# Performance work log

Hardware: AMD Instinct MI355X
Metric: run time of the kernel (lower is better)

The kernel has to match this reference:

```python
import jax, jax.numpy as jnp
import numpy as np

NUM_HEADS = 16
D_MODEL = 1024
D_K = 64
D_V = 64
B, S = 4, 2048
TEMPERATURE = float(np.sqrt(NUM_HEADS * D_K))  # module uses sqrt(H*d_k), not sqrt(d_k)


def setup_inputs() -> dict:
    key = jax.random.key(0)
    ks = jax.random.split(key, 7)
    q = jax.random.normal(ks[0], (B, S, D_MODEL), dtype=jnp.float32)
    k = jax.random.normal(ks[1], (B, S, D_MODEL), dtype=jnp.float32)
    v = jax.random.normal(ks[2], (B, S, D_MODEL), dtype=jnp.float32)
    # causal mask: True = masked out (matches torch masked_fill semantics)
    mask = jnp.broadcast_to(jnp.triu(jnp.ones((S, S), dtype=bool), k=1), (B, S, S))
    scale = 1.0 / np.sqrt(D_MODEL)
    Wq = jax.random.normal(ks[3], (D_MODEL, NUM_HEADS * D_K), dtype=jnp.float32) * scale
    Wk = jax.random.normal(ks[4], (D_MODEL, NUM_HEADS * D_K), dtype=jnp.float32) * scale
    Wv = jax.random.normal(ks[5], (D_MODEL, NUM_HEADS * D_V), dtype=jnp.float32) * scale
    Wo = jax.random.normal(ks[6], (NUM_HEADS * D_V, D_MODEL), dtype=jnp.float32) * scale
    return {"q": q, "k": k, "v": v, "mask": mask,
            "Wq": Wq, "Wk": Wk, "Wv": Wv, "Wo": Wo}


def _split_heads(x):
    # [B,S,H*d] -> [B,H,S,d]
    b, s, _ = x.shape
    return x.reshape(b, s, NUM_HEADS, -1).transpose(0, 2, 1, 3)


def reference(q, k, v, mask, Wq, Wk, Wv, Wo):
    qh = _split_heads(q @ Wq)   # [B,H,S,d_k]
    kh = _split_heads(k @ Wk)   # [B,H,S,d_k]
    vh = _split_heads(v @ Wv)   # [B,H,S,d_v]
    attn = jnp.einsum('bhqd,bhkd->bhqk', qh / TEMPERATURE, kh)
    attn = jnp.where(mask[:, None, :, :], -jnp.inf, attn)
    attn = jax.nn.softmax(attn, axis=-1)
    out = jnp.einsum('bhqk,bhkd->bhqd', attn, vh)  # [B,H,S,d_v]
    out = out.transpose(0, 2, 1, 3).reshape(q.shape[0], q.shape[1], -1)
    out = out @ Wo  # [B,S,d_model]
    return out, attn
```

## Files before the change

kernel.cpp:

```cpp
#include <hip/hip_runtime.h>
#include <hip/hip_bf16.h>
#include <math.h>

#define SLEN 2048
#define NB 4
#define NH 16
#define DM 1024
#define DH 64

typedef __attribute__((ext_vector_type(8))) short bf16x8;
typedef __attribute__((ext_vector_type(8))) unsigned short ushort8;
typedef __attribute__((ext_vector_type(4))) unsigned short ushort4v;
typedef __attribute__((ext_vector_type(4))) float f32x4;

#define MFMA16(a, b, c) __builtin_amdgcn_mfma_f32_16x16x32_bf16((a), (b), (c), 0, 0, 0)

__device__ __forceinline__ unsigned short f2b(float f) {
    unsigned u = __builtin_bit_cast(unsigned, f);
    u = (u + 0x7FFFu + ((u >> 16) & 1u)) >> 16;
    return (unsigned short)u;
}

__device__ __forceinline__ float b2f(unsigned short h) {
    return __builtin_bit_cast(float, (unsigned)h << 16);
}

__device__ __forceinline__ void gload16(const unsigned short* g, unsigned short* l) {
    __builtin_amdgcn_global_load_lds((const __attribute__((address_space(1))) unsigned int*)g,
                                     (__attribute__((address_space(3))) unsigned int*)l,
                                     16, 0, 0);
}

__global__ __launch_bounds__(256) void wtrans4(const float* __restrict__ w0,
                                               const float* __restrict__ w1,
                                               const float* __restrict__ w2,
                                               const float* __restrict__ w3,
                                               unsigned short* __restrict__ outBase) {
    int z = blockIdx.z;
    const float* in = (z == 0) ? w0 : (z == 1) ? w1 : (z == 2) ? w2 : w3;
    unsigned short* out = outBase + (size_t)z * DM * DM;
    float scale = (z == 0) ? (1.4426950408889634f / 32.f) : 1.f;
    __shared__ float tile[32][33];
    int k0 = blockIdx.y * 32, n0 = blockIdx.x * 32;
    int tx = threadIdx.x & 31, ty = threadIdx.x >> 5;
    for (int i = ty; i < 32; i += 8) tile[i][tx] = in[(size_t)(k0 + i) * DM + n0 + tx];
    __syncthreads();
    for (int i = ty; i < 32; i += 8) out[(size_t)(n0 + i) * DM + k0 + tx] = f2b(tile[tx][i] * scale);
}

__global__ __launch_bounds__(256) void cast3(const float* __restrict__ q,
                                             const float* __restrict__ k,
                                             const float* __restrict__ v,
                                             unsigned short* __restrict__ dstBase, int n8) {
    int z = blockIdx.z;
    const float* in = (z == 0) ? q : (z == 1) ? k : v;
    unsigned short* out = dstBase + (size_t)z * NB * SLEN * DM;
    int stride = gridDim.x * 256;
    for (int i = blockIdx.x * 256 + threadIdx.x; i < n8; i += stride) {
        float4 a = ((const float4*)in)[2 * i];
        float4 b = ((const float4*)in)[2 * i + 1];
        ushort8 h = {f2b(a.x), f2b(a.y), f2b(a.z), f2b(a.w),
                     f2b(b.x), f2b(b.y), f2b(b.z), f2b(b.w)};
        ((ushort8*)out)[i] = h;
    }
}

__global__ __launch_bounds__(256) void vtrans(const unsigned short* __restrict__ Vh,
                                              unsigned short* __restrict__ Vt) {
    int bh = blockIdx.y;
    int b = bh >> 4, h = bh & 15;
    int s0 = blockIdx.x * 64;
    __shared__ __align__(16) unsigned short tile[64][72];
    int t = threadIdx.x;
    int r = t >> 2, seg = (t & 3) * 16;
    const ushort8* src = (const ushort8*)&Vh[(size_t)(b * SLEN + s0 + r) * DM + h * 64 + seg];
    *(ushort8*)&tile[r][seg] = src[0];
    *(ushort8*)&tile[r][seg + 8] = src[1];
    __syncthreads();
    unsigned short tmp[16];
#pragma unroll
    for (int i = 0; i < 16; i++) tmp[i] = tile[seg + i][r];
    ushort8 o0, o1;
#pragma unroll
    for (int i = 0; i < 8; i++) { o0[i] = tmp[i]; o1[i] = tmp[8 + i]; }
    unsigned short* dst = &Vt[(size_t)(bh * 64 + r) * SLEN + s0 + seg];
    *(ushort8*)dst = o0;
    *(ushort8*)&dst[8] = o1;
}

template <bool OUT_F32>
__global__ __launch_bounds__(256) void gemm_mz(const unsigned short* __restrict__ A0, size_t sA,
                                               const unsigned short* __restrict__ B0, size_t sB,
                                               void* __restrict__ C0, size_t sC,
                                               int N, int K) {
    __shared__ __align__(16) unsigned short As[128 * 64];
    __shared__ __align__(16) unsigned short Bs[128 * 64];
    int bid = blockIdx.x;
    int z = bid >> 9, inner = bid & 511;
    const unsigned short* A = A0 + (size_t)z * sA;
    const unsigned short* Bt = B0 + (size_t)z * sB;
    int m0 = (inner >> 3) * 128, n0 = (inner & 7) * 128;
    int t = threadIdx.x, lane = t & 63, w = t >> 6;
    int wm = (w >> 1) * 64, wn = (w & 1) * 64;
    int lr = lane & 15, hi = lane >> 4, lk = hi * 8, lq = hi * 4;
    int srow = w * 8 + (lane >> 3);
    int scol = (lane & 7) * 8;
    f32x4 acc[4][4] = {};
    for (int kt = 0; kt < K; kt += 64) {
        __syncthreads();
#pragma unroll
        for (int c = 0; c < 4; c++) {
            int row = c * 32 + srow;
            gload16(&A[(size_t)(m0 + row) * K + kt + scol], &As[(c * 4 + w) * 512]);
            gload16(&Bt[(size_t)(n0 + row) * K + kt + scol], &Bs[(c * 4 + w) * 512]);
        }
        __syncthreads();
#pragma unroll
        for (int ks = 0; ks < 2; ks++) {
            bf16x8 a[4], b[4];
#pragma unroll
            for (int mt = 0; mt < 4; mt++) a[mt] = *(const bf16x8*)&As[(wm + mt * 16 + lr) * 64 + ks * 32 + lk];
#pragma unroll
            for (int nt = 0; nt < 4; nt++) b[nt] = *(const bf16x8*)&Bs[(wn + nt * 16 + lr) * 64 + ks * 32 + lk];
#pragma unroll
            for (int mt = 0; mt < 4; mt++)
#pragma unroll
                for (int nt = 0; nt < 4; nt++) acc[mt][nt] = MFMA16(a[mt], b[nt], acc[mt][nt]);
        }
    }
#pragma unroll
    for (int mt = 0; mt < 4; mt++)
#pragma unroll
        for (int nt = 0; nt < 4; nt++)
#pragma unroll
            for (int r = 0; r < 4; r++) {
                int rr = m0 + wm + mt * 16 + lq + r;
                int cc = n0 + wn + nt * 16 + lr;
                if constexpr (OUT_F32)
                    ((float*)C0 + (size_t)z * sC)[(size_t)rr * N + cc] = acc[mt][nt][r];
                else
                    ((unsigned short*)C0 + (size_t)z * sC)[(size_t)rr * N + cc] = f2b(acc[mt][nt][r]);
            }
}

__global__ __launch_bounds__(512) void attn_kernel(const unsigned short* __restrict__ Qh,
                                                   const unsigned short* __restrict__ Kh,
                                                   const unsigned short* __restrict__ Vt,
                                                   float* __restrict__ attn_out,
                                                   unsigned short* __restrict__ O) {
    int bx = blockIdx.x;
    int qt = bx >> 6, bh = bx & 63;
    int b = bh >> 4, h = bh & 15;
    int q0 = qt * 128;
    int t = threadIdx.x, lane = t & 63, w = t >> 6;
    int lr = lane & 15, hi = lane >> 4, lk = hi * 8, lq = hi * 4;
    __shared__ __align__(16) unsigned short Ks[2][64 * 72];
    __shared__ __align__(16) unsigned short Vs[64 * 72];
    __shared__ __align__(16) unsigned short Ps[8][16 * 72];

    int qrow = q0 + w * 16 + lr;
    bf16x8 aq0 = *(const bf16x8*)&Qh[(size_t)(b * SLEN + qrow) * DM + h * 64 + lk];
    bf16x8 aq1 = *(const bf16x8*)&Qh[(size_t)(b * SLEN + qrow) * DM + h * 64 + 32 + lk];

    int srow = t >> 3, sseg = (t & 7) * 8;
    int ntile = 2 * qt + 2;
    int nfull = (q0 + w * 16 + 1) >> 6;
    int nact  = ((q0 + w * 16 + 15) >> 6) + 1;
    const unsigned short* Kbase = &Kh[(size_t)(b * SLEN + srow) * DM + h * 64 + sseg];
    const unsigned short* Vbase = &Vt[(size_t)(bh * 64 + srow) * SLEN + sseg];

    float rowsum = 0.f;

    ushort8 kreg = *(const ushort8*)&Kbase[0];
    for (int j = 0; j < ntile; j++) {
        ushort8 knext{};
        if (j + 1 < ntile) knext = *(const ushort8*)&Kbase[(size_t)(j + 1) * 64 * DM];
        *(ushort8*)&Ks[j & 1][srow * 72 + sseg] = kreg;
        __syncthreads();
        kreg = knext;
        if (j < nact) {
            const unsigned short* Kb = Ks[j & 1];
            if (j < nfull) {
#pragma unroll
                for (int nt = 0; nt < 4; nt++) {
                    f32x4 acc = {0.f, 0.f, 0.f, 0.f};
                    bf16x8 b0 = *(const bf16x8*)&Kb[(nt * 16 + lr) * 72 + lk];
                    bf16x8 b1 = *(const bf16x8*)&Kb[(nt * 16 + lr) * 72 + 32 + lk];
                    acc = MFMA16(b0, aq0, acc);
                    acc = MFMA16(b1, aq1, acc);
#pragma unroll
                    for (int r = 0; r < 4; r++) rowsum += exp2f(acc[r]);
                }
            } else {
#pragma unroll
                for (int nt = 0; nt < 4; nt++) {
                    f32x4 acc = {0.f, 0.f, 0.f, 0.f};
                    bf16x8 b0 = *(const bf16x8*)&Kb[(nt * 16 + lr) * 72 + lk];
                    bf16x8 b1 = *(const bf16x8*)&Kb[(nt * 16 + lr) * 72 + 32 + lk];
                    acc = MFMA16(b0, aq0, acc);
                    acc = MFMA16(b1, aq1, acc);
#pragma unroll
                    for (int r = 0; r < 4; r++) {
                        int key = j * 64 + nt * 16 + lq + r;
                        if (key <= qrow) rowsum += exp2f(acc[r]);
                    }
                }
            }
        }
    }
    rowsum += __shfl_xor(rowsum, 16);
    rowsum += __shfl_xor(rowsum, 32);
    float nlg = -log2f(rowsum);
    f32x4 cinit = {nlg, nlg, nlg, nlg};

    f32x4 acco[4] = {};
    kreg = *(const ushort8*)&Kbase[0];
    ushort8 vreg = *(const ushort8*)&Vbase[0];
    for (int j = 0; j < ntile; j++) {
        ushort8 knext{}, vnext{};
        if (j + 1 < ntile) {
            knext = *(const ushort8*)&Kbase[(size_t)(j + 1) * 64 * DM];
            vnext = *(const ushort8*)&Vbase[(j + 1) * 64];
        }
        __syncthreads();
        *(ushort8*)&Ks[0][srow * 72 + sseg] = kreg;
        *(ushort8*)&Vs[srow * 72 + sseg] = vreg;
        __syncthreads();
        kreg = knext;
        vreg = vnext;
        if (j >= nact) continue;
        bool full = j < nfull;
#pragma unroll
        for (int nt = 0; nt < 4; nt++) {
            f32x4 acc = cinit;
            bf16x8 b0 = *(const bf16x8*)&Ks[0][(nt * 16 + lr) * 72 + lk];
            bf16x8 b1 = *(const bf16x8*)&Ks[0][(nt * 16 + lr) * 72 + 32 + lk];
            acc = MFMA16(b0, aq0, acc);
            acc = MFMA16(b1, aq1, acc);
            ushort4v pb;
            if (full) {
#pragma unroll
                for (int r = 0; r < 4; r++)
                    pb[r] = (unsigned short)(__builtin_bit_cast(unsigned, exp2f(acc[r])) >> 16);
            } else {
#pragma unroll
                for (int r = 0; r < 4; r++) {
                    int key = j * 64 + nt * 16 + lq + r;
                    float p = (key <= qrow) ? exp2f(acc[r]) : 0.f;
                    pb[r] = (unsigned short)(__builtin_bit_cast(unsigned, p) >> 16);
                }
            }
            *(ushort4v*)&Ps[w][lr * 72 + nt * 16 + lq] = pb;
        }
        {
            size_t abase = ((size_t)bh * SLEN + q0 + w * 16) * SLEN + j * 64 + lr * 4;
#pragma unroll
            for (int i = 0; i < 4; i++) {
                int row = i * 4 + hi;
                ushort4v pb4 = *(const ushort4v*)&Ps[w][row * 72 + lr * 4];
                f32x4 pf = {b2f(pb4[0]), b2f(pb4[1]), b2f(pb4[2]), b2f(pb4[3])};
                __builtin_nontemporal_store(pf, (f32x4*)&attn_out[abase + (size_t)row * SLEN]);
            }
        }
        bf16x8 pa0 = *(const bf16x8*)&Ps[w][lr * 72 + lk];
        bf16x8 pa1 = *(const bf16x8*)&Ps[w][lr * 72 + 32 + lk];
#pragma unroll
        for (int nt = 0; nt < 4; nt++) {
            bf16x8 bv0 = *(const bf16x8*)&Vs[(nt * 16 + lr) * 72 + lk];
            bf16x8 bv1 = *(const bf16x8*)&Vs[(nt * 16 + lr) * 72 + 32 + lk];
            acco[nt] = MFMA16(pa0, bv0, acco[nt]);
            acco[nt] = MFMA16(pa1, bv1, acco[nt]);
        }
    }

    int kz = nact * 64;
    if (kz < SLEN) {
        int n4 = (SLEN - kz) >> 2;
        f32x4 z4 = {0.f, 0.f, 0.f, 0.f};
        for (int rr = 0; rr < 16; rr++) {
            int qr = q0 + w * 16 + rr;
            f32x4* dst = (f32x4*)&attn_out[((size_t)bh * SLEN + qr) * SLEN + kz];
            for (int i = lane; i < n4; i += 64) __builtin_nontemporal_store(z4, &dst[i]);
        }
    }

#pragma unroll
    for (int nt = 0; nt < 4; nt++)
#pragma unroll
        for (int r = 0; r < 4; r++) {
            int qr = q0 + w * 16 + lq + r;
            O[(size_t)(b * SLEN + qr) * DM + h * 64 + nt * 16 + lr] = f2b(acco[nt][r]);
        }
}

extern "C" void kernel_launch(void* const* d_in, const int* in_sizes, int n_in,
                              void* d_out, int out_size, void* d_ws, size_t ws_size,
                              hipStream_t stream) {
    const float* q = (const float*)d_in[0];
    const float* k = (const float*)d_in[1];
    const float* v = (const float*)d_in[2];
    const float* Wq = (const float*)d_in[4];
    const float* Wk = (const float*)d_in[5];
    const float* Wv = (const float*)d_in[6];
    const float* Wo = (const float*)d_in[7];

    const size_t WSZ = (size_t)DM * DM;
    const size_t MSZ = (size_t)NB * SLEN * DM;

    unsigned short* WqT = (unsigned short*)d_ws;
    unsigned short* WoT = WqT + 3 * WSZ;
    unsigned short* Qh  = WqT + 4 * WSZ;
    unsigned short* Kh  = Qh + MSZ;
    unsigned short* Vh  = Kh + MSZ;
    unsigned short* Vt  = Vh + MSZ;
    unsigned short* O   = Vt + MSZ;

    float* out = (float*)d_out;
    float* attn = out + MSZ;
    unsigned short* Cq = (unsigned short*)attn;

    wtrans4<<<dim3(32, 32, 4), 256, 0, stream>>>(Wq, Wk, Wv, Wo, WqT);

    const int n8 = (int)(MSZ / 8);
    cast3<<<dim3(1024, 1, 3), 256, 0, stream>>>(q, k, v, Cq, n8);

    gemm_mz<false><<<1536, 256, 0, stream>>>(Cq, MSZ, WqT, WSZ, (void*)Qh, MSZ, DM, DM);

    vtrans<<<dim3(SLEN / 64, NB * NH), 256, 0, stream>>>(Vh, Vt);

    attn_kernel<<<NB * NH * (SLEN / 128), 512, 0, stream>>>(Qh, Kh, Vt, attn, O);

    gemm_mz<true><<<512, 256, 0, stream>>>(O, 0, WoT, 0, d_out, 0, DM, DM);
}
```

Before: 405.1 us.

## Load K and V MFMA fragments directly from global memory, dropping LDS staging

The attention kernel no longer stages K and V tiles through shared memory with block-wide barriers. Each wave now reads its MFMA operand fragments straight from global memory and loops only over its own active key tiles (nact) instead of the block-wide tile count. This removes the __syncthreads calls and the LDS traffic, and lets waves with fewer causal tiles finish early. The cost is that all 8 waves fetch the same K/V data separately, relying on the L1/L2 caches, and the loads are no longer prefetched a tile ahead.

```diff
diff --git a/kernel.cpp b/kernel.cpp
--- a/kernel.cpp
+++ b/kernel.cpp
@@ -154,56 +154,37 @@
     int q0 = qt * 128;
     int t = threadIdx.x, lane = t & 63, w = t >> 6;
     int lr = lane & 15, hi = lane >> 4, lk = hi * 8, lq = hi * 4;
-    __shared__ __align__(16) unsigned short Ks[2][64 * 72];
-    __shared__ __align__(16) unsigned short Vs[64 * 72];
     __shared__ __align__(16) unsigned short Ps[8][16 * 72];
 
     int qrow = q0 + w * 16 + lr;
     bf16x8 aq0 = *(const bf16x8*)&Qh[(size_t)(b * SLEN + qrow) * DM + h * 64 + lk];
     bf16x8 aq1 = *(const bf16x8*)&Qh[(size_t)(b * SLEN + qrow) * DM + h * 64 + 32 + lk];
 
-    int srow = t >> 3, sseg = (t & 7) * 8;
-    int ntile = 2 * qt + 2;
     int nfull = (q0 + w * 16 + 1) >> 6;
     int nact  = ((q0 + w * 16 + 15) >> 6) + 1;
-    const unsigned short* Kbase = &Kh[(size_t)(b * SLEN + srow) * DM + h * 64 + sseg];
-    const unsigned short* Vbase = &Vt[(size_t)(bh * 64 + srow) * SLEN + sseg];
+    const unsigned short* Kfrag = &Kh[(size_t)(b * SLEN + lr) * DM + h * 64 + lk];
+    const unsigned short* Vfrag = &Vt[(size_t)(bh * 64 + lr) * SLEN + lk];
 
     float rowsum = 0.f;
 
-    ushort8 kreg = *(const ushort8*)&Kbase[0];
-    for (int j = 0; j < ntile; j++) {
-        ushort8 knext{};
-        if (j + 1 < ntile) knext = *(const ushort8*)&Kbase[(size_t)(j + 1) * 64 * DM];
-        *(ushort8*)&Ks[j & 1][srow * 72 + sseg] = kreg;
-        __syncthreads();
-        kreg = knext;
-        if (j < nact) {
-            const unsigned short* Kb = Ks[j & 1];
-            if (j < nfull) {
-#pragma unroll
-                for (int nt = 0; nt < 4; nt++) {
-                    f32x4 acc = {0.f, 0.f, 0.f, 0.f};
-                    bf16x8 b0 = *(const bf16x8*)&Kb[(nt * 16 + lr) * 72 + lk];
-                    bf16x8 b1 = *(const bf16x8*)&Kb[(nt * 16 + lr) * 72 + 32 + lk];
-                    acc = MFMA16(b0, aq0, acc);
-                    acc = MFMA16(b1, aq1, acc);
-#pragma unroll
-                    for (int r = 0; r < 4; r++) rowsum += exp2f(acc[r]);
-                }
+    for (int j = 0; j < nact; j++) {
+        bool full = j < nfull;
+#pragma unroll
+        for (int nt = 0; nt < 4; nt++) {
+            const unsigned short* kp = &Kfrag[(size_t)(j * 64 + nt * 16) * DM];
+            bf16x8 b0 = *(const bf16x8*)kp;
+            bf16x8 b1 = *(const bf16x8*)&kp[32];
+            f32x4 acc = {0.f, 0.f, 0.f, 0.f};
+            acc = MFMA16(b0, aq0, acc);
+            acc = MFMA16(b1, aq1, acc);
+            if (full) {
+#pragma unroll
+                for (int r = 0; r < 4; r++) rowsum += exp2f(acc[r]);
             } else {
 #pragma unroll
-                for (int nt = 0; nt < 4; nt++) {
-                    f32x4 acc = {0.f, 0.f, 0.f, 0.f};
-                    bf16x8 b0 = *(const bf16x8*)&Kb[(nt * 16 + lr) * 72 + lk];
-                    bf16x8 b1 = *(const bf16x8*)&Kb[(nt * 16 + lr) * 72 + 32 + lk];
-                    acc = MFMA16(b0, aq0, acc);
-                    acc = MFMA16(b1, aq1, acc);
-#pragma unroll
-                    for (int r = 0; r < 4; r++) {
-                        int key = j * 64 + nt * 16 + lq + r;
-                        if (key <= qrow) rowsum += exp2f(acc[r]);
-                    }
+                for (int r = 0; r < 4; r++) {
+                    int key = j * 64 + nt * 16 + lq + r;
+                    if (key <= qrow) rowsum += exp2f(acc[r]);
                 }
             }
         }
@@ -214,27 +195,14 @@
     f32x4 cinit = {nlg, nlg, nlg, nlg};
 
     f32x4 acco[4] = {};
-    kreg = *(const ushort8*)&Kbase[0];
-    ushort8 vreg = *(const ushort8*)&Vbase[0];
-    for (int j = 0; j < ntile; j++) {
-        ushort8 knext{}, vnext{};
-        if (j + 1 < ntile) {
-            knext = *(const ushort8*)&Kbase[(size_t)(j + 1) * 64 * DM];
-            vnext = *(const ushort8*)&Vbase[(j + 1) * 64];
-        }
-        __syncthreads();
-        *(ushort8*)&Ks[0][srow * 72 + sseg] = kreg;
-        *(ushort8*)&Vs[srow * 72 + sseg] = vreg;
-        __syncthreads();
-        kreg = knext;
-        vreg = vnext;
-        if (j >= nact) continue;
+    for (int j = 0; j < nact; j++) {
         bool full = j < nfull;
 #pragma unroll
         for (int nt = 0; nt < 4; nt++) {
+            const unsigned short* kp = &Kfrag[(size_t)(j * 64 + nt * 16) * DM];
+            bf16x8 b0 = *(const bf16x8*)kp;
+            bf16x8 b1 = *(const bf16x8*)&kp[32];
             f32x4 acc = cinit;
-            bf16x8 b0 = *(const bf16x8*)&Ks[0][(nt * 16 + lr) * 72 + lk];
-            bf16x8 b1 = *(const bf16x8*)&Ks[0][(nt * 16 + lr) * 72 + 32 + lk];
             acc = MFMA16(b0, aq0, acc);
             acc = MFMA16(b1, aq1, acc);
             ushort4v pb;
@@ -266,8 +234,9 @@
         bf16x8 pa1 = *(const bf16x8*)&Ps[w][lr * 72 + 32 + lk];
 #pragma unroll
         for (int nt = 0; nt < 4; nt++) {
-            bf16x8 bv0 = *(const bf16x8*)&Vs[(nt * 16 + lr) * 72 + lk];
-            bf16x8 bv1 = *(const bf16x8*)&Vs[(nt * 16 + lr) * 72 + 32 + lk];
+            const unsigned short* vp = &Vfrag[(size_t)(nt * 16) * SLEN + j * 64];
+            bf16x8 bv0 = *(const bf16x8*)vp;
+            bf16x8 bv1 = *(const bf16x8*)&vp[32];
             acco[nt] = MFMA16(pa0, bv0, acco[nt]);
             acco[nt] = MFMA16(pa1, bv1, acco[nt]);
         }
```

Result: slower. 600.6 us (+48.3%).

## Fuse fp32-to-bf16 cast and V transpose into QKV projection GEMM

Applied to the files above, without the earlier changes.

Removes the separate cast kernel by having the QKV GEMM load fp32 activations, convert them to bf16 in registers and store them into shared memory, with register prefetch of the next K tile. For the V projection, MFMA operands are swapped so the output is written directly in transposed [h*64+d][b*S+s] layout, removing the vtrans kernel. The attention kernel's V addressing is updated to match. This cuts two launches and several full activation round-trips through memory. In exchange, the A loads now go through registers instead of direct-to-LDS loads, and the transposed V stores are strided.

```diff
diff --git a/kernel.cpp b/kernel.cpp
--- a/kernel.cpp
+++ b/kernel.cpp
@@ -48,57 +48,21 @@
     for (int i = ty; i < 32; i += 8) out[(size_t)(n0 + i) * DM + k0 + tx] = f2b(tile[tx][i] * scale);
 }
 
-__global__ __launch_bounds__(256) void cast3(const float* __restrict__ q,
-                                             const float* __restrict__ k,
-                                             const float* __restrict__ v,
-                                             unsigned short* __restrict__ dstBase, int n8) {
-    int z = blockIdx.z;
-    const float* in = (z == 0) ? q : (z == 1) ? k : v;
-    unsigned short* out = dstBase + (size_t)z * NB * SLEN * DM;
-    int stride = gridDim.x * 256;
-    for (int i = blockIdx.x * 256 + threadIdx.x; i < n8; i += stride) {
-        float4 a = ((const float4*)in)[2 * i];
-        float4 b = ((const float4*)in)[2 * i + 1];
-        ushort8 h = {f2b(a.x), f2b(a.y), f2b(a.z), f2b(a.w),
-                     f2b(b.x), f2b(b.y), f2b(b.z), f2b(b.w)};
-        ((ushort8*)out)[i] = h;
-    }
-}
-
-__global__ __launch_bounds__(256) void vtrans(const unsigned short* __restrict__ Vh,
-                                              unsigned short* __restrict__ Vt) {
-    int bh = blockIdx.y;
-    int b = bh >> 4, h = bh & 15;
-    int s0 = blockIdx.x * 64;
-    __shared__ __align__(16) unsigned short tile[64][72];
-    int t = threadIdx.x;
-    int r = t >> 2, seg = (t & 3) * 16;
-    const ushort8* src = (const ushort8*)&Vh[(size_t)(b * SLEN + s0 + r) * DM + h * 64 + seg];
-    *(ushort8*)&tile[r][seg] = src[0];
-    *(ushort8*)&tile[r][seg + 8] = src[1];
-    __syncthreads();
-    unsigned short tmp[16];
-#pragma unroll
-    for (int i = 0; i < 16; i++) tmp[i] = tile[seg + i][r];
-    ushort8 o0, o1;
-#pragma unroll
-    for (int i = 0; i < 8; i++) { o0[i] = tmp[i]; o1[i] = tmp[8 + i]; }
-    unsigned short* dst = &Vt[(size_t)(bh * 64 + r) * SLEN + s0 + seg];
-    *(ushort8*)dst = o0;
-    *(ushort8*)&dst[8] = o1;
-}
-
-template <bool OUT_F32>
-__global__ __launch_bounds__(256) void gemm_mz(const unsigned short* __restrict__ A0, size_t sA,
-                                               const unsigned short* __restrict__ B0, size_t sB,
-                                               void* __restrict__ C0, size_t sC,
-                                               int N, int K) {
+__global__ __launch_bounds__(256) void gemm_qkv(const float* __restrict__ Aq,
+                                                const float* __restrict__ Ak,
+                                                const float* __restrict__ Av,
+                                                const unsigned short* __restrict__ B0,
+                                                unsigned short* __restrict__ C0) {
+    const size_t WSZ = (size_t)DM * DM;
+    const size_t MSZ = (size_t)NB * SLEN * DM;
     __shared__ __align__(16) unsigned short As[128 * 64];
     __shared__ __align__(16) unsigned short Bs[128 * 64];
     int bid = blockIdx.x;
     int z = bid >> 9, inner = bid & 511;
-    const unsigned short* A = A0 + (size_t)z * sA;
-    const unsigned short* Bt = B0 + (size_t)z * sB;
+    const float* Af = (z == 0) ? Aq : (z == 1) ? Ak : Av;
+    const unsigned short* Bt = B0 + (size_t)z * WSZ;
+    unsigned short* C = C0 + (size_t)z * MSZ;
+    bool ct = (z == 2);
     int m0 = (inner >> 3) * 128, n0 = (inner & 7) * 128;
     int t = threadIdx.x, lane = t & 63, w = t >> 6;
     int wm = (w >> 1) * 64, wn = (w & 1) * 64;
@@ -106,13 +70,106 @@
     int srow = w * 8 + (lane >> 3);
     int scol = (lane & 7) * 8;
     f32x4 acc[4][4] = {};
-    for (int kt = 0; kt < K; kt += 64) {
+    float4 pf[4][2];
+#pragma unroll
+    for (int c = 0; c < 4; c++) {
+        const float* ap = &Af[(size_t)(m0 + c * 32 + srow) * DM + scol];
+        pf[c][0] = ((const float4*)ap)[0];
+        pf[c][1] = ((const float4*)ap)[1];
+    }
+    for (int kt = 0; kt < DM; kt += 64) {
         __syncthreads();
 #pragma unroll
         for (int c = 0; c < 4; c++) {
             int row = c * 32 + srow;
-            gload16(&A[(size_t)(m0 + row) * K + kt + scol], &As[(c * 4 + w) * 512]);
-            gload16(&Bt[(size_t)(n0 + row) * K + kt + scol], &Bs[(c * 4 + w) * 512]);
+            float4 f0 = pf[c][0], f1 = pf[c][1];
+            ushort8 h = {f2b(f0.x), f2b(f0.y), f2b(f0.z), f2b(f0.w),
+                         f2b(f1.x), f2b(f1.y), f2b(f1.z), f2b(f1.w)};
+            *(ushort8*)&As[row * 64 + scol] = h;
+            gload16(&Bt[(size_t)(n0 + row) * DM + kt + scol], &Bs[(c * 4 + w) * 512]);
+        }
+        __syncthreads();
+        if (kt + 64 < DM) {
+#pragma unroll
+            for (int c = 0; c < 4; c++) {
+                const float* ap = &Af[(size_t)(m0 + c * 32 + srow) * DM + kt + 64 + scol];
+                pf[c][0] = ((const float4*)ap)[0];
+                pf[c][1] = ((const float4*)ap)[1];
+            }
+        }
+        if (ct) {
+#pragma unroll
+            for (int ks = 0; ks < 2; ks++) {
+                bf16x8 a[4], b[4];
+#pragma unroll
+                for (int mt = 0; mt < 4; mt++) a[mt] = *(const bf16x8*)&As[(wm + mt * 16 + lr) * 64 + ks * 32 + lk];
+#pragma unroll
+                for (int nt = 0; nt < 4; nt++) b[nt] = *(const bf16x8*)&Bs[(wn + nt * 16 + lr) * 64 + ks * 32 + lk];
+#pragma unroll
+                for (int mt = 0; mt < 4; mt++)
+#pragma unroll
+                    for (int nt = 0; nt < 4; nt++) acc[mt][nt] = MFMA16(b[nt], a[mt], acc[mt][nt]);
+            }
+        } else {
+#pragma unroll
+            for (int ks = 0; ks < 2; ks++) {
+                bf16x8 a[4], b[4];
+#pragma unroll
+                for (int mt = 0; mt < 4; mt++) a[mt] = *(const bf16x8*)&As[(wm + mt * 16 + lr) * 64 + ks * 32 + lk];
+#pragma unroll
+                for (int nt = 0; nt < 4; nt++) b[nt] = *(const bf16x8*)&Bs[(wn + nt * 16 + lr) * 64 + ks * 32 + lk];
+#pragma unroll
+                for (int mt = 0; mt < 4; mt++)
+#pragma unroll
+                    for (int nt = 0; nt < 4; nt++) acc[mt][nt] = MFMA16(a[mt], b[nt], acc[mt][nt]);
+            }
+        }
+    }
+    if (ct) {
+#pragma unroll
+        for (int mt = 0; mt < 4; mt++)
+#pragma unroll
+            for (int nt = 0; nt < 4; nt++)
+#pragma unroll
+                for (int r = 0; r < 4; r++) {
+                    int rr = n0 + wn + nt * 16 + lq + r;
+                    int cc = m0 + wm + mt * 16 + lr;
+                    C[(size_t)rr * (NB * SLEN) + cc] = f2b(acc[mt][nt][r]);
+                }
+    } else {
+#pragma unroll
+        for (int mt = 0; mt < 4; mt++)
+#pragma unroll
+            for (int nt = 0; nt < 4; nt++)
+#pragma unroll
+                for (int r = 0; r < 4; r++) {
+                    int rr = m0 + wm + mt * 16 + lq + r;
+                    int cc = n0 + wn + nt * 16 + lr;
+                    C[(size_t)rr * DM + cc] = f2b(acc[mt][nt][r]);
+                }
+    }
+}
+
+__global__ __launch_bounds__(256) void gemm_o(const unsigned short* __restrict__ A,
+                                              const unsigned short* __restrict__ Bt,
+                                              float* __restrict__ Cf) {
+    __shared__ __align__(16) unsigned short As[128 * 64];
+    __shared__ __align__(16) unsigned short Bs[128 * 64];
+    int inner = blockIdx.x;
+    int m0 = (inner >> 3) * 128, n0 = (inner & 7) * 128;
+    int t = threadIdx.x, lane = t & 63, w = t >> 6;
+    int wm = (w >> 1) * 64, wn = (w & 1) * 64;
+    int lr = lane & 15, hi = lane >> 4, lk = hi * 8, lq = hi * 4;
+    int srow = w * 8 + (lane >> 3);
+    int scol = (lane & 7) * 8;
+    f32x4 acc[4][4] = {};
+    for (int kt = 0; kt < DM; kt += 64) {
+        __syncthreads();
+#pragma unroll
+        for (int c = 0; c < 4; c++) {
+            int row = c * 32 + srow;
+            gload16(&A[(size_t)(m0 + row) * DM + kt + scol], &As[(c * 4 + w) * 512]);
+            gload16(&Bt[(size_t)(n0 + row) * DM + kt + scol], &Bs[(c * 4 + w) * 512]);
         }
         __syncthreads();
 #pragma unroll
@@ -136,10 +193,7 @@
             for (int r = 0; r < 4; r++) {
                 int rr = m0 + wm + mt * 16 + lq + r;
                 int cc = n0 + wn + nt * 16 + lr;
-                if constexpr (OUT_F32)
-                    ((float*)C0 + (size_t)z * sC)[(size_t)rr * N + cc] = acc[mt][nt][r];
-                else
-                    ((unsigned short*)C0 + (size_t)z * sC)[(size_t)rr * N + cc] = f2b(acc[mt][nt][r]);
+                Cf[(size_t)rr * DM + cc] = acc[mt][nt][r];
             }
 }
 
@@ -167,7 +221,7 @@
     int nfull = (q0 + w * 16 + 1) >> 6;
     int nact  = ((q0 + w * 16 + 15) >> 6) + 1;
     const unsigned short* Kbase = &Kh[(size_t)(b * SLEN + srow) * DM + h * 64 + sseg];
-    const unsigned short* Vbase = &Vt[(size_t)(bh * 64 + srow) * SLEN + sseg];
+    const unsigned short* Vbase = &Vt[(size_t)(h * 64 + srow) * (NB * SLEN) + b * SLEN + sseg];
 
     float rowsum = 0.f;
 
@@ -311,24 +365,17 @@
     unsigned short* WoT = WqT + 3 * WSZ;
     unsigned short* Qh  = WqT + 4 * WSZ;
     unsigned short* Kh  = Qh + MSZ;
-    unsigned short* Vh  = Kh + MSZ;
-    unsigned short* Vt  = Vh + MSZ;
+    unsigned short* Vt  = Kh + MSZ;
     unsigned short* O   = Vt + MSZ;
 
     float* out = (float*)d_out;
     float* attn = out + MSZ;
-    unsigned short* Cq = (unsigned short*)attn;
 
     wtrans4<<<dim3(32, 32, 4), 256, 0, stream>>>(Wq, Wk, Wv, Wo, WqT);
 
-    const int n8 = (int)(MSZ / 8);
-    cast3<<<dim3(1024, 1, 3), 256, 0, stream>>>(q, k, v, Cq, n8);
-
-    gemm_mz<false><<<1536, 256, 0, stream>>>(Cq, MSZ, WqT, WSZ, (void*)Qh, MSZ, DM, DM);
-
-    vtrans<<<dim3(SLEN / 64, NB * NH), 256, 0, stream>>>(Vh, Vt);
+    gemm_qkv<<<1536, 256, 0, stream>>>(q, k, v, WqT, Qh);
 
     attn_kernel<<<NB * NH * (SLEN / 128), 512, 0, stream>>>(Qh, Kh, Vt, attn, O);
 
-    gemm_mz<true><<<512, 256, 0, stream>>>(O, 0, WoT, 0, d_out, 0, DM, DM);
-}
+    gemm_o<<<512, 256, 0, stream>>>(O, WoT, out);
+}
```

Measured after the change: 469.7 us. +15.9%, slower.

## Fuse V transpose into projection GEMM epilogue and reverse attention tile order

Applied to the files above, without the earlier changes.

The V projection GEMM now computes the transposed product by swapping its MFMA operands and writes V directly in [H*64, B*S] layout, so the separate vtrans kernel and its intermediate buffer go away. The attention kernel reads V from this new layout and processes query tiles in reverse order, so the longest causal tiles are scheduled first. The transposed epilogue writes rows strided by B*S, which may coalesce less well. The fused transpose saves a kernel launch and a full read and write of V, and the reordering is meant to reduce tail imbalance.

```diff
diff --git a/kernel.cpp b/kernel.cpp
--- a/kernel.cpp
+++ b/kernel.cpp
@@ -65,40 +65,18 @@
     }
 }
 
-__global__ __launch_bounds__(256) void vtrans(const unsigned short* __restrict__ Vh,
-                                              unsigned short* __restrict__ Vt) {
-    int bh = blockIdx.y;
-    int b = bh >> 4, h = bh & 15;
-    int s0 = blockIdx.x * 64;
-    __shared__ __align__(16) unsigned short tile[64][72];
-    int t = threadIdx.x;
-    int r = t >> 2, seg = (t & 3) * 16;
-    const ushort8* src = (const ushort8*)&Vh[(size_t)(b * SLEN + s0 + r) * DM + h * 64 + seg];
-    *(ushort8*)&tile[r][seg] = src[0];
-    *(ushort8*)&tile[r][seg + 8] = src[1];
-    __syncthreads();
-    unsigned short tmp[16];
-#pragma unroll
-    for (int i = 0; i < 16; i++) tmp[i] = tile[seg + i][r];
-    ushort8 o0, o1;
-#pragma unroll
-    for (int i = 0; i < 8; i++) { o0[i] = tmp[i]; o1[i] = tmp[8 + i]; }
-    unsigned short* dst = &Vt[(size_t)(bh * 64 + r) * SLEN + s0 + seg];
-    *(ushort8*)dst = o0;
-    *(ushort8*)&dst[8] = o1;
-}
-
 template <bool OUT_F32>
 __global__ __launch_bounds__(256) void gemm_mz(const unsigned short* __restrict__ A0, size_t sA,
                                                const unsigned short* __restrict__ B0, size_t sB,
                                                void* __restrict__ C0, size_t sC,
-                                               int N, int K) {
+                                               int N, int K, int vct) {
     __shared__ __align__(16) unsigned short As[128 * 64];
     __shared__ __align__(16) unsigned short Bs[128 * 64];
     int bid = blockIdx.x;
     int z = bid >> 9, inner = bid & 511;
     const unsigned short* A = A0 + (size_t)z * sA;
     const unsigned short* Bt = B0 + (size_t)z * sB;
+    bool ct = vct && (z == 2);
     int m0 = (inner >> 3) * 128, n0 = (inner & 7) * 128;
     int t = threadIdx.x, lane = t & 63, w = t >> 6;
     int wm = (w >> 1) * 64, wn = (w & 1) * 64;
@@ -115,32 +93,61 @@
             gload16(&Bt[(size_t)(n0 + row) * K + kt + scol], &Bs[(c * 4 + w) * 512]);
         }
         __syncthreads();
-#pragma unroll
-        for (int ks = 0; ks < 2; ks++) {
-            bf16x8 a[4], b[4];
-#pragma unroll
-            for (int mt = 0; mt < 4; mt++) a[mt] = *(const bf16x8*)&As[(wm + mt * 16 + lr) * 64 + ks * 32 + lk];
-#pragma unroll
-            for (int nt = 0; nt < 4; nt++) b[nt] = *(const bf16x8*)&Bs[(wn + nt * 16 + lr) * 64 + ks * 32 + lk];
-#pragma unroll
-            for (int mt = 0; mt < 4; mt++)
-#pragma unroll
-                for (int nt = 0; nt < 4; nt++) acc[mt][nt] = MFMA16(a[mt], b[nt], acc[mt][nt]);
-        }
-    }
-#pragma unroll
-    for (int mt = 0; mt < 4; mt++)
-#pragma unroll
-        for (int nt = 0; nt < 4; nt++)
-#pragma unroll
-            for (int r = 0; r < 4; r++) {
-                int rr = m0 + wm + mt * 16 + lq + r;
-                int cc = n0 + wn + nt * 16 + lr;
-                if constexpr (OUT_F32)
-                    ((float*)C0 + (size_t)z * sC)[(size_t)rr * N + cc] = acc[mt][nt][r];
-                else
-                    ((unsigned short*)C0 + (size_t)z * sC)[(size_t)rr * N + cc] = f2b(acc[mt][nt][r]);
-            }
+        if (ct) {
+#pragma unroll
+            for (int ks = 0; ks < 2; ks++) {
+                bf16x8 a[4], b[4];
+#pragma unroll
+                for (int mt = 0; mt < 4; mt++) a[mt] = *(const bf16x8*)&As[(wm + mt * 16 + lr) * 64 + ks * 32 + lk];
+#pragma unroll
+                for (int nt = 0; nt < 4; nt++) b[nt] = *(const bf16x8*)&Bs[(wn + nt * 16 + lr) * 64 + ks * 32 + lk];
+#pragma unroll
+                for (int mt = 0; mt < 4; mt++)
+#pragma unroll
+                    for (int nt = 0; nt < 4; nt++) acc[mt][nt] = MFMA16(b[nt], a[mt], acc[mt][nt]);
+            }
+        } else {
+#pragma unroll
+            for (int ks = 0; ks < 2; ks++) {
+                bf16x8 a[4], b[4];
+#pragma unroll
+                for (int mt = 0; mt < 4; mt++) a[mt] = *(const bf16x8*)&As[(wm + mt * 16 + lr) * 64 + ks * 32 + lk];
+#pragma unroll
+                for (int nt = 0; nt < 4; nt++) b[nt] = *(const bf16x8*)&Bs[(wn + nt * 16 + lr) * 64 + ks * 32 + lk];
+#pragma unroll
+                for (int mt = 0; mt < 4; mt++)
+#pragma unroll
+                    for (int nt = 0; nt < 4; nt++) acc[mt][nt] = MFMA16(a[mt], b[nt], acc[mt][nt]);
+            }
+        }
+    }
+    if (ct) {
+        unsigned short* C = (unsigned short*)C0 + (size_t)z * sC;
+#pragma unroll
+        for (int mt = 0; mt < 4; mt++)
+#pragma unroll
+            for (int nt = 0; nt < 4; nt++)
+#pragma unroll
+                for (int r = 0; r < 4; r++) {
+                    int rr = n0 + wn + nt * 16 + lq + r;
+                    int cc = m0 + wm + mt * 16 + lr;
+                    C[(size_t)rr * (NB * SLEN) + cc] = f2b(acc[mt][nt][r]);
+                }
+    } else {
+#pragma unroll
+        for (int mt = 0; mt < 4; mt++)
+#pragma unroll
+            for (int nt = 0; nt < 4; nt++)
+#pragma unroll
+                for (int r = 0; r < 4; r++) {
+                    int rr = m0 + wm + mt * 16 + lq + r;
+                    int cc = n0 + wn + nt * 16 + lr;
+                    if constexpr (OUT_F32)
+                        ((float*)C0 + (size_t)z * sC)[(size_t)rr * N + cc] = acc[mt][nt][r];
+                    else
+                        ((unsigned short*)C0 + (size_t)z * sC)[(size_t)rr * N + cc] = f2b(acc[mt][nt][r]);
+                }
+    }
 }
 
 __global__ __launch_bounds__(512) void attn_kernel(const unsigned short* __restrict__ Qh,
@@ -149,7 +156,8 @@
                                                    float* __restrict__ attn_out,
                                                    unsigned short* __restrict__ O) {
     int bx = blockIdx.x;
-    int qt = bx >> 6, bh = bx & 63;
+    int qt = 15 - (bx >> 6);
+    int bh = bx & 63;
     int b = bh >> 4, h = bh & 15;
     int q0 = qt * 128;
     int t = threadIdx.x, lane = t & 63, w = t >> 6;
@@ -167,7 +175,7 @@
     int nfull = (q0 + w * 16 + 1) >> 6;
     int nact  = ((q0 + w * 16 + 15) >> 6) + 1;
     const unsigned short* Kbase = &Kh[(size_t)(b * SLEN + srow) * DM + h * 64 + sseg];
-    const unsigned short* Vbase = &Vt[(size_t)(bh * 64 + srow) * SLEN + sseg];
+    const unsigned short* Vbase = &Vt[(size_t)(h * 64 + srow) * (NB * SLEN) + b * SLEN + sseg];
 
     float rowsum = 0.f;
 
@@ -311,8 +319,7 @@
     unsigned short* WoT = WqT + 3 * WSZ;
     unsigned short* Qh  = WqT + 4 * WSZ;
     unsigned short* Kh  = Qh + MSZ;
-    unsigned short* Vh  = Kh + MSZ;
-    unsigned short* Vt  = Vh + MSZ;
+    unsigned short* Vt  = Kh + MSZ;
     unsigned short* O   = Vt + MSZ;
 
     float* out = (float*)d_out;
@@ -324,11 +331,9 @@
     const int n8 = (int)(MSZ / 8);
     cast3<<<dim3(1024, 1, 3), 256, 0, stream>>>(q, k, v, Cq, n8);
 
-    gemm_mz<false><<<1536, 256, 0, stream>>>(Cq, MSZ, WqT, WSZ, (void*)Qh, MSZ, DM, DM);
-
-    vtrans<<<dim3(SLEN / 64, NB * NH), 256, 0, stream>>>(Vh, Vt);
+    gemm_mz<false><<<1536, 256, 0, stream>>>(Cq, MSZ, WqT, WSZ, (void*)Qh, MSZ, DM, DM, 1);
 
     attn_kernel<<<NB * NH * (SLEN / 128), 512, 0, stream>>>(Qh, Kh, Vt, attn, O);
 
-    gemm_mz<true><<<512, 256, 0, stream>>>(O, 0, WoT, 0, d_out, 0, DM, DM);
-}
+    gemm_mz<true><<<512, 256, 0, stream>>>(O, 0, WoT, 0, d_out, 0, DM, DM, 0);
+}
```

Measured after the change: 440.9 us. 8.8% more time.
